# Kernel optimization log

Measured on AMD Instinct MI355X. Metric: run time of the kernel, lower is better.

Reference implementation:

```python
import jax, jax.numpy as jnp
import numpy as np

B, N, D_IN, D_OUT = 4, 2048, 1024, 1024


def setup_inputs() -> dict:
    key = jax.random.key(0)
    k0, k1, k2, k3 = jax.random.split(key, 4)
    x = jax.random.normal(k0, (B, N, D_IN), dtype=jnp.float32)
    # torch Linear weight is [out, in]; store transposed [in, out] for x @ W
    W_query = jax.random.normal(k1, (D_IN, D_OUT), dtype=jnp.float32) * (D_IN ** -0.5)
    W_key = jax.random.normal(k2, (D_IN, D_OUT), dtype=jnp.float32) * (D_IN ** -0.5)
    W_value = jax.random.normal(k3, (D_IN, D_OUT), dtype=jnp.float32) * (D_IN ** -0.5)
    return {"x": x, "W_query": W_query, "W_key": W_key, "W_value": W_value}


def reference(x, W_query, W_key, W_value):
    # x: [B, N, D_IN]
    num_tokens = x.shape[1]
    embed_dim = x.shape[2]  # NB: original scales by INPUT embed dim
    q = jnp.einsum('bnd,de->bne', x, W_query)  # [B, N, D_OUT]
    k = jnp.einsum('bnd,de->bne', x, W_key)
    v = jnp.einsum('bnd,de->bne', x, W_value)
    scores = jnp.einsum('bqe,bke->bqk', q, k)  # [B, N, N]
    idx = jnp.arange(num_tokens)
    causal_mask = idx[None, :] > idx[:, None]  # True above diagonal
    scores = jnp.where(causal_mask[None, :, :], -jnp.inf, scores)
    scale = jnp.asarray(embed_dim, scores.dtype) ** 0.5
    attn = jax.nn.softmax(scores / scale, axis=-1)  # dropout p=0 (eval)
    context = jnp.einsum('bqk,bke->bqe', attn, v)  # [B, N, D_OUT]
    return context
```

## Files before the change

### kernel.cpp

```cpp
#include <hip/hip_runtime.h>


typedef __attribute__((ext_vector_type(8))) _Float16 half8;
typedef __attribute__((ext_vector_type(4))) _Float16 half4v;
typedef __attribute__((ext_vector_type(4))) float floatx4;

#define AS1 __attribute__((address_space(1)))
#define AS3 __attribute__((address_space(3)))

__device__ __forceinline__ void load16_lds(void* lds, const void* g) {
  __builtin_amdgcn_global_load_lds((AS1 void*)g, (AS3 void*)lds, 16, 0, 0);
}


__global__ __launch_bounds__(256)
void conv_f32_f16(const float* __restrict__ in, _Float16* __restrict__ out,
                  float* __restrict__ l) {
  if (blockIdx.x < 8192) {
    const int i = (blockIdx.x * 256 + threadIdx.x) << 2;
    float4 v = *(const float4*)(in + i);
    half4v o = { (_Float16)v.x, (_Float16)v.y, (_Float16)v.z, (_Float16)v.w };
    *(half4v*)(out + i) = o;
  } else {
    const int i = ((blockIdx.x - 8192) * 256 + threadIdx.x) << 2;
    *(float4*)(l + i) = float4{0.f, 0.f, 0.f, 0.f};
  }
}

__global__ __launch_bounds__(256)
void transpose_w(const float* __restrict__ W0, const float* __restrict__ W1,
                 const float* __restrict__ W2, _Float16* __restrict__ Wt) {
  const float* W = blockIdx.z == 0 ? W0 : (blockIdx.z == 1 ? W1 : W2);
  _Float16* out = Wt + (long long)blockIdx.z * 1048576;
  __shared__ _Float16 t[32][33];
  const int tx = threadIdx.x, ty = threadIdx.y;
  const int n0 = blockIdx.x << 5, k0 = blockIdx.y << 5;
#pragma unroll
  for (int i = 0; i < 4; ++i)
    t[ty + i * 8][tx] = (_Float16)W[(long long)(k0 + ty + i * 8) * 1024 + n0 + tx];
  __syncthreads();
#pragma unroll
  for (int i = 0; i < 4; ++i)
    out[(long long)(n0 + ty + i * 8) * 1024 + k0 + tx] = t[tx][ty + i * 8];
}

__global__ __launch_bounds__(256)
void gemm_qkv(const _Float16* __restrict__ A, const _Float16* __restrict__ B,
              _Float16* __restrict__ Q, _Float16* __restrict__ Kh,
              _Float16* __restrict__ Vt) {
  const int bm = blockIdx.y, bn = blockIdx.x;
  const _Float16* Ab = A + (long long)bm * 128 * 1024;
  const _Float16* Bb = B + (long long)bn * 128 * 1024;

  __shared__ _Float16 As[128][64];
  __shared__ _Float16 Bs[128][64];

  const int tid = threadIdx.x;
  const int wave = tid >> 6, lane = tid & 63;
  const int quad = lane >> 4, lr = lane & 15;
  const int wm = (wave >> 1) << 6, wn = (wave & 1) << 6;
  const int srow = lane >> 3;
  const int goff = ((lane & 7) ^ srow) << 3;

  floatx4 acc[4][4] = {};
  const _Float16* ga = Ab + (long long)(wave * 8 + srow) * 1024 + goff;
  const _Float16* gb = Bb + (long long)(wave * 8 + srow) * 1024 + goff;

  for (int k0 = 0; k0 < 1024; k0 += 64) {
    __syncthreads();
#pragma unroll
    for (int c = 0; c < 4; ++c) {
      load16_lds(&As[wave * 8 + 32 * c][0], ga + c * 32 * 1024);
      load16_lds(&Bs[wave * 8 + 32 * c][0], gb + c * 32 * 1024);
    }
    ga += 64; gb += 64;
    __syncthreads();

#pragma unroll
    for (int kk = 0; kk < 2; ++kk) {
      half8 af[4], bf[4];
#pragma unroll
      for (int i = 0; i < 4; ++i) {
        const int ra = wm + (i << 4) + lr;
        const int rb = wn + (i << 4) + lr;
        af[i] = *(const half8*)&As[ra][(((kk << 2) + quad) ^ (ra & 7)) << 3];
        bf[i] = *(const half8*)&Bs[rb][(((kk << 2) + quad) ^ (rb & 7)) << 3];
      }
#pragma unroll
      for (int i = 0; i < 4; ++i)
#pragma unroll
        for (int j = 0; j < 4; ++j)
          acc[i][j] = __builtin_amdgcn_mfma_f32_16x16x32_f16(af[i], bf[j], acc[i][j], 0, 0, 0);
    }
  }

  const int colb = bn * 128 + wn + lr;
  const int rowb = bm * 128 + wm + (quad << 2);

  if (bn < 16) {
    _Float16* C = (bn < 8) ? Q : Kh;
    const int cb = colb & 1023;
#pragma unroll
    for (int i = 0; i < 4; ++i)
#pragma unroll
      for (int j = 0; j < 4; ++j)
#pragma unroll
        for (int r = 0; r < 4; ++r)
          C[(long long)(rowb + (i << 4) + r) * 1024 + cb + (j << 4)] =
              (_Float16)acc[i][j][r];
  } else {
    const int b = rowb >> 11;
    const int tb = rowb & 2047;
#pragma unroll
    for (int i = 0; i < 4; ++i) {
      const int tok = tb + (i << 4);
#pragma unroll
      for (int j = 0; j < 4; ++j) {
        const int d = (colb & 1023) + (j << 4);
        half4v v = { (_Float16)acc[i][j][0], (_Float16)acc[i][j][1],
                     (_Float16)acc[i][j][2], (_Float16)acc[i][j][3] };
        *(half4v*)&Vt[(long long)b * 2097152 + (long long)d * 2048 + tok] = v;
      }
    }
  }
}

__global__ __launch_bounds__(256)
void gemm_s_exp(const _Float16* __restrict__ Q, const _Float16* __restrict__ Kh,
                _Float16* __restrict__ P, float* __restrict__ l) {
  int t = blockIdx.x;
  const int bz = blockIdx.y;
  int bm = 0;
  for (;;) { const int c = (bm >> 2) + 1; if (t < c) break; t -= c; ++bm; }
  const int bn = t;

  const _Float16* Ab = Q  + (long long)bz * 2097152 + (long long)bm * 64 * 1024;
  const _Float16* Bb = Kh + (long long)bz * 2097152 + (long long)bn * 256 * 1024;
  const int nmaxl = bm * 64 + 63 - bn * 256;

  __shared__ _Float16 As[64][64];
  __shared__ _Float16 Bs[256][64];

  const int tid = threadIdx.x;
  const int wave = tid >> 6, lane = tid & 63;
  const int quad = lane >> 4, lr = lane & 15;
  const int srow = lane >> 3;
  const int goff = ((lane & 7) ^ srow) << 3;

  floatx4 acc[4][4] = {};
  const _Float16* ga = Ab + (long long)(wave * 16 + srow) * 1024 + goff;
  const _Float16* gb = Bb + (long long)(wave * 64 + srow) * 1024 + goff;

  for (int k0 = 0; k0 < 1024; k0 += 64) {
    __syncthreads();
    load16_lds(&As[wave * 16][0],     ga);
    load16_lds(&As[wave * 16 + 8][0], ga + 8 * 1024);
#pragma unroll
    for (int c = 0; c < 8; ++c)
      if (wave * 64 + 8 * c <= nmaxl)
        load16_lds(&Bs[wave * 64 + 8 * c][0], gb + c * 8 * 1024);
    ga += 64; gb += 64;
    __syncthreads();

#pragma unroll
    for (int kk = 0; kk < 2; ++kk) {
      half8 af[4], bf[4];
#pragma unroll
      for (int i = 0; i < 4; ++i) {
        const int ra = (i << 4) + lr;
        af[i] = *(const half8*)&As[ra][(((kk << 2) + quad) ^ (ra & 7)) << 3];
      }
#pragma unroll
      for (int j = 0; j < 4; ++j)
        if (wave * 64 + (j << 4) <= nmaxl) {
          const int rb = wave * 64 + (j << 4) + lr;
          bf[j] = *(const half8*)&Bs[rb][(((kk << 2) + quad) ^ (rb & 7)) << 3];
        }
#pragma unroll
      for (int i = 0; i < 4; ++i)
#pragma unroll
        for (int j = 0; j < 4; ++j)
          if (wave * 64 + (j << 4) <= nmaxl)
            acc[i][j] = __builtin_amdgcn_mfma_f32_16x16x32_f16(af[i], bf[j], acc[i][j], 0, 0, 0);
    }
  }

  const int n0 = bn * 256 + wave * 64;
  const int rowq = bm * 64 + (quad << 2);
  _Float16* Pb = P + (long long)bz * 4194304;
  const float scl = 0.03125f;

  float rs[4][4];
#pragma unroll
  for (int i = 0; i < 4; ++i)
#pragma unroll
    for (int r = 0; r < 4; ++r) rs[i][r] = 0.f;

#pragma unroll
  for (int j = 0; j < 4; ++j)
    if (wave * 64 + (j << 4) <= nmaxl) {
      const int kcol = n0 + (j << 4) + lr;
#pragma unroll
      for (int i = 0; i < 4; ++i)
#pragma unroll
        for (int r = 0; r < 4; ++r) {
          const int q = rowq + (i << 4) + r;
          const float p = (kcol <= q) ? __expf(acc[i][j][r] * scl) : 0.f;
          Pb[(long long)q * 2048 + kcol] = (_Float16)p;
          rs[i][r] += p;
        }
    }

#pragma unroll
  for (int i = 0; i < 4; ++i)
#pragma unroll
    for (int r = 0; r < 4; ++r) {
#pragma unroll
      for (int off = 1; off < 16; off <<= 1)
        rs[i][r] += __shfl_xor(rs[i][r], off);
    }
  if (lr == 0) {
    float* lb = l + bz * 2048;
#pragma unroll
    for (int i = 0; i < 4; ++i)
#pragma unroll
      for (int r = 0; r < 4; ++r)
        atomicAdd(&lb[rowq + (i << 4) + r], rs[i][r]);
  }
}

__global__ __launch_bounds__(256)
void gemm_pv(const _Float16* __restrict__ P, const _Float16* __restrict__ Vt,
             const float* __restrict__ l, float* __restrict__ out) {
  const int bn = blockIdx.x, bz = blockIdx.z;
  const int bm = 31 - blockIdx.y;
  const int Keff = 64 * (bm + 1);

  const _Float16* Ab = P  + (long long)bz * 4194304 + (long long)bm * 64 * 2048;
  const _Float16* Bb = Vt + (long long)bz * 2097152 + (long long)bn * 256 * 2048;

  __shared__ _Float16 As[64][64];
  __shared__ _Float16 Bs[256][64];

  const int tid = threadIdx.x;
  const int wave = tid >> 6, lane = tid & 63;
  const int quad = lane >> 4, lr = lane & 15;
  const int srow = lane >> 3;
  const int goff = ((lane & 7) ^ srow) << 3;

  floatx4 acc[4][4] = {};
  const _Float16* ga = Ab + (long long)(wave * 16 + srow) * 2048 + goff;
  const _Float16* gb = Bb + (long long)(wave * 64 + srow) * 2048 + goff;

  for (int k0 = 0; k0 < Keff; k0 += 64) {
    __syncthreads();
    load16_lds(&As[wave * 16][0],     ga);
    load16_lds(&As[wave * 16 + 8][0], ga + 8 * 2048);
#pragma unroll
    for (int c = 0; c < 8; ++c)
      load16_lds(&Bs[wave * 64 + 8 * c][0], gb + c * 8 * 2048);
    ga += 64; gb += 64;
    __syncthreads();

#pragma unroll
    for (int kk = 0; kk < 2; ++kk) {
      half8 af[4], bf[4];
#pragma unroll
      for (int i = 0; i < 4; ++i) {
        const int ra = (i << 4) + lr;
        af[i] = *(const half8*)&As[ra][(((kk << 2) + quad) ^ (ra & 7)) << 3];
      }
#pragma unroll
      for (int j = 0; j < 4; ++j) {
        const int rb = wave * 64 + (j << 4) + lr;
        bf[j] = *(const half8*)&Bs[rb][(((kk << 2) + quad) ^ (rb & 7)) << 3];
      }
#pragma unroll
      for (int i = 0; i < 4; ++i)
#pragma unroll
        for (int j = 0; j < 4; ++j)
          acc[i][j] = __builtin_amdgcn_mfma_f32_16x16x32_f16(af[i], bf[j], acc[i][j], 0, 0, 0);
    }
  }

  const int d0 = bn * 256 + wave * 64;
  const int rowq = bm * 64 + (quad << 2);
  const float* lb = l + bz * 2048;
  float* Cb = out + (long long)bz * 2097152;

  float linv[4][4];
#pragma unroll
  for (int i = 0; i < 4; ++i)
#pragma unroll
    for (int r = 0; r < 4; ++r)
      linv[i][r] = 1.0f / lb[rowq + (i << 4) + r];

#pragma unroll
  for (int i = 0; i < 4; ++i)
#pragma unroll
    for (int j = 0; j < 4; ++j)
#pragma unroll
      for (int r = 0; r < 4; ++r)
        Cb[(long long)(rowq + (i << 4) + r) * 1024 + d0 + (j << 4) + lr] =
            acc[i][j][r] * linv[i][r];
}


extern "C" void kernel_launch(void* const* d_in, const int* in_sizes, int n_in,
                              void* d_out, int out_size, void* d_ws, size_t ws_size,
                              hipStream_t stream) {
  const float* x  = (const float*)d_in[0];
  const float* Wq = (const float*)d_in[1];
  const float* Wk = (const float*)d_in[2];
  const float* Wv = (const float*)d_in[3];
  float* out = (float*)d_out;

  char* ws = (char*)d_ws;
  _Float16* xh = (_Float16*)(ws);
  _Float16* Wt = (_Float16*)(ws + 16777216);
  _Float16* Q  = (_Float16*)(ws + 23068672);
  _Float16* Kh = (_Float16*)(ws + 39845888);
  _Float16* Vt = (_Float16*)(ws + 56623104);
  _Float16* P  = (_Float16*)(ws + 73400320);
  float*    l  = (float*)   (ws + 106954752);

  conv_f32_f16<<<8200, 256, 0, stream>>>(x, xh, l);
  transpose_w<<<dim3(32, 32, 3), dim3(32, 8), 0, stream>>>(Wq, Wk, Wv, Wt);

  gemm_qkv<<<dim3(24, 64), 256, 0, stream>>>(xh, Wt, Q, Kh, Vt);

  gemm_s_exp<<<dim3(144, 4), 256, 0, stream>>>(Q, Kh, P, l);

  gemm_pv<<<dim3(4, 32, 4), 256, 0, stream>>>(P, Vt, l, out);
}
```

Baseline: 252.0 us.

## Double-buffer LDS tiles with K=32 stages in QK and PV GEMMs

Both attention GEMM kernels now split the shared-memory tiles into two buffers of K=32 and issue the next stage's direct-to-LDS global loads before computing on the current one. The aim is to overlap global memory latency with MFMA work and to cut the two barriers per iteration down to one. The swizzle pattern changes to suit 32-wide rows. The trade-off is twice as many loop iterations, each doing half the MFMA work. There is also a risk that the single barrier does not order the asynchronous LDS loads correctly without an explicit vmcnt wait.

```diff
diff --git a/kernel.cpp b/kernel.cpp
--- a/kernel.cpp
+++ b/kernel.cpp
@@ -138,51 +138,52 @@
   const _Float16* Bb = Kh + (long long)bz * 2097152 + (long long)bn * 256 * 1024;
   const int nmaxl = bm * 64 + 63 - bn * 256;
 
-  __shared__ _Float16 As[64][64];
-  __shared__ _Float16 Bs[256][64];
+  __shared__ _Float16 As[2][64][32];
+  __shared__ _Float16 Bs[2][256][32];
 
   const int tid = threadIdx.x;
   const int wave = tid >> 6, lane = tid & 63;
   const int quad = lane >> 4, lr = lane & 15;
-  const int srow = lane >> 3;
-  const int goff = ((lane & 7) ^ srow) << 3;
+  const int srow = lane >> 2;
+  const int goff = ((lane & 3) ^ ((srow >> 1) & 3)) << 3;
+
+  const _Float16* ga = Ab + (long long)(16 * wave + srow) * 1024 + goff;
+  const _Float16* gb = Bb + (long long)(64 * wave + srow) * 1024 + goff;
 
   floatx4 acc[4][4] = {};
-  const _Float16* ga = Ab + (long long)(wave * 16 + srow) * 1024 + goff;
-  const _Float16* gb = Bb + (long long)(wave * 64 + srow) * 1024 + goff;
-
-  for (int k0 = 0; k0 < 1024; k0 += 64) {
+
+  auto stage = [&](int buf, int kof) {
+    load16_lds(&As[buf][16 * wave][0], ga + kof);
+#pragma unroll
+    for (int c = 0; c < 4; ++c)
+      if (64 * wave + 16 * c <= nmaxl)
+        load16_lds(&Bs[buf][64 * wave + 16 * c][0], gb + 16 * c * 1024 + kof);
+  };
+
+  stage(0, 0);
+  for (int it = 0; it < 32; ++it) {
     __syncthreads();
-    load16_lds(&As[wave * 16][0],     ga);
-    load16_lds(&As[wave * 16 + 8][0], ga + 8 * 1024);
-#pragma unroll
-    for (int c = 0; c < 8; ++c)
-      if (wave * 64 + 8 * c <= nmaxl)
-        load16_lds(&Bs[wave * 64 + 8 * c][0], gb + c * 8 * 1024);
-    ga += 64; gb += 64;
-    __syncthreads();
-
-#pragma unroll
-    for (int kk = 0; kk < 2; ++kk) {
-      half8 af[4], bf[4];
-#pragma unroll
-      for (int i = 0; i < 4; ++i) {
-        const int ra = (i << 4) + lr;
-        af[i] = *(const half8*)&As[ra][(((kk << 2) + quad) ^ (ra & 7)) << 3];
+    if (it + 1 < 32) stage((it + 1) & 1, (it + 1) * 32);
+    const int buf = it & 1;
+
+    half8 af[4], bf[4];
+#pragma unroll
+    for (int i = 0; i < 4; ++i) {
+      const int ra = (i << 4) + lr;
+      af[i] = *(const half8*)&As[buf][ra][(quad ^ ((ra >> 1) & 3)) << 3];
+    }
+#pragma unroll
+    for (int j = 0; j < 4; ++j)
+      if (64 * wave + (j << 4) <= nmaxl) {
+        const int rb = 64 * wave + (j << 4) + lr;
+        bf[j] = *(const half8*)&Bs[buf][rb][(quad ^ ((rb >> 1) & 3)) << 3];
       }
 #pragma unroll
+    for (int i = 0; i < 4; ++i)
+#pragma unroll
       for (int j = 0; j < 4; ++j)
-        if (wave * 64 + (j << 4) <= nmaxl) {
-          const int rb = wave * 64 + (j << 4) + lr;
-          bf[j] = *(const half8*)&Bs[rb][(((kk << 2) + quad) ^ (rb & 7)) << 3];
-        }
-#pragma unroll
-      for (int i = 0; i < 4; ++i)
-#pragma unroll
-        for (int j = 0; j < 4; ++j)
-          if (wave * 64 + (j << 4) <= nmaxl)
-            acc[i][j] = __builtin_amdgcn_mfma_f32_16x16x32_f16(af[i], bf[j], acc[i][j], 0, 0, 0);
-    }
+        if (64 * wave + (j << 4) <= nmaxl)
+          acc[i][j] = __builtin_amdgcn_mfma_f32_16x16x32_f16(af[i], bf[j], acc[i][j], 0, 0, 0);
   }
 
   const int n0 = bn * 256 + wave * 64;
@@ -234,53 +235,54 @@
              const float* __restrict__ l, float* __restrict__ out) {
   const int bn = blockIdx.x, bz = blockIdx.z;
   const int bm = 31 - blockIdx.y;
-  const int Keff = 64 * (bm + 1);
+  const int niter = 2 * (bm + 1);
 
   const _Float16* Ab = P  + (long long)bz * 4194304 + (long long)bm * 64 * 2048;
   const _Float16* Bb = Vt + (long long)bz * 2097152 + (long long)bn * 256 * 2048;
 
-  __shared__ _Float16 As[64][64];
-  __shared__ _Float16 Bs[256][64];
+  __shared__ _Float16 As[2][64][32];
+  __shared__ _Float16 Bs[2][256][32];
 
   const int tid = threadIdx.x;
   const int wave = tid >> 6, lane = tid & 63;
   const int quad = lane >> 4, lr = lane & 15;
-  const int srow = lane >> 3;
-  const int goff = ((lane & 7) ^ srow) << 3;
+  const int srow = lane >> 2;
+  const int goff = ((lane & 3) ^ ((srow >> 1) & 3)) << 3;
+
+  const _Float16* ga = Ab + (long long)(16 * wave + srow) * 2048 + goff;
+  const _Float16* gb = Bb + (long long)(64 * wave + srow) * 2048 + goff;
 
   floatx4 acc[4][4] = {};
-  const _Float16* ga = Ab + (long long)(wave * 16 + srow) * 2048 + goff;
-  const _Float16* gb = Bb + (long long)(wave * 64 + srow) * 2048 + goff;
-
-  for (int k0 = 0; k0 < Keff; k0 += 64) {
+
+  auto stage = [&](int buf, int kof) {
+    load16_lds(&As[buf][16 * wave][0], ga + kof);
+#pragma unroll
+    for (int c = 0; c < 4; ++c)
+      load16_lds(&Bs[buf][64 * wave + 16 * c][0], gb + 16 * c * 2048 + kof);
+  };
+
+  stage(0, 0);
+  for (int it = 0; it < niter; ++it) {
     __syncthreads();
-    load16_lds(&As[wave * 16][0],     ga);
-    load16_lds(&As[wave * 16 + 8][0], ga + 8 * 2048);
-#pragma unroll
-    for (int c = 0; c < 8; ++c)
-      load16_lds(&Bs[wave * 64 + 8 * c][0], gb + c * 8 * 2048);
-    ga += 64; gb += 64;
-    __syncthreads();
-
-#pragma unroll
-    for (int kk = 0; kk < 2; ++kk) {
-      half8 af[4], bf[4];
-#pragma unroll
-      for (int i = 0; i < 4; ++i) {
-        const int ra = (i << 4) + lr;
-        af[i] = *(const half8*)&As[ra][(((kk << 2) + quad) ^ (ra & 7)) << 3];
-      }
-#pragma unroll
-      for (int j = 0; j < 4; ++j) {
-        const int rb = wave * 64 + (j << 4) + lr;
-        bf[j] = *(const half8*)&Bs[rb][(((kk << 2) + quad) ^ (rb & 7)) << 3];
-      }
-#pragma unroll
-      for (int i = 0; i < 4; ++i)
-#pragma unroll
-        for (int j = 0; j < 4; ++j)
-          acc[i][j] = __builtin_amdgcn_mfma_f32_16x16x32_f16(af[i], bf[j], acc[i][j], 0, 0, 0);
-    }
+    if (it + 1 < niter) stage((it + 1) & 1, (it + 1) * 32);
+    const int buf = it & 1;
+
+    half8 af[4], bf[4];
+#pragma unroll
+    for (int i = 0; i < 4; ++i) {
+      const int ra = (i << 4) + lr;
+      af[i] = *(const half8*)&As[buf][ra][(quad ^ ((ra >> 1) & 3)) << 3];
+    }
+#pragma unroll
+    for (int j = 0; j < 4; ++j) {
+      const int rb = 64 * wave + (j << 4) + lr;
+      bf[j] = *(const half8*)&Bs[buf][rb][(quad ^ ((rb >> 1) & 3)) << 3];
+    }
+#pragma unroll
+    for (int i = 0; i < 4; ++i)
+#pragma unroll
+      for (int j = 0; j < 4; ++j)
+        acc[i][j] = __builtin_amdgcn_mfma_f32_16x16x32_f16(af[i], bf[j], acc[i][j], 0, 0, 0);
   }
 
   const int d0 = bn * 256 + wave * 64;
```

After: 270.3 us. 1.07x slower.

## Retile score and PV GEMMs to square 128x128 blocks with 2x2 wave layout

Applied to the files above, without the earlier changes.

Both attention GEMMs move from 64x256 block tiles with one wave per 64-column strip to 128x128 tiles split into a 2x2 grid of waves. Each wave now holds a 64x64 output sub-tile. The aim is a better balance of LDS loads between the A and B operands and more operand reuse per byte loaded. The trade-off is coarser causal skipping: the per-wave masked-tile pruning in the score kernel is removed, so diagonal blocks compute some fully masked work, and the PV kernel has fewer, larger blocks.

```diff
diff --git a/kernel.cpp b/kernel.cpp
--- a/kernel.cpp
+++ b/kernel.cpp
@@ -129,36 +129,35 @@
 void gemm_s_exp(const _Float16* __restrict__ Q, const _Float16* __restrict__ Kh,
                 _Float16* __restrict__ P, float* __restrict__ l) {
   int t = blockIdx.x;
+  int bm = 0;
+  for (;;) { const int c = bm + 1; if (t < c) break; t -= c; ++bm; }
+  const int bn = t;
   const int bz = blockIdx.y;
-  int bm = 0;
-  for (;;) { const int c = (bm >> 2) + 1; if (t < c) break; t -= c; ++bm; }
-  const int bn = t;
-
-  const _Float16* Ab = Q  + (long long)bz * 2097152 + (long long)bm * 64 * 1024;
-  const _Float16* Bb = Kh + (long long)bz * 2097152 + (long long)bn * 256 * 1024;
-  const int nmaxl = bm * 64 + 63 - bn * 256;
-
-  __shared__ _Float16 As[64][64];
-  __shared__ _Float16 Bs[256][64];
+
+  const _Float16* Ab = Q  + (long long)bz * 2097152 + (long long)bm * 128 * 1024;
+  const _Float16* Bb = Kh + (long long)bz * 2097152 + (long long)bn * 128 * 1024;
+
+  __shared__ _Float16 As[128][64];
+  __shared__ _Float16 Bs[128][64];
 
   const int tid = threadIdx.x;
   const int wave = tid >> 6, lane = tid & 63;
   const int quad = lane >> 4, lr = lane & 15;
+  const int wm = (wave >> 1) << 6, wn = (wave & 1) << 6;
   const int srow = lane >> 3;
   const int goff = ((lane & 7) ^ srow) << 3;
 
   floatx4 acc[4][4] = {};
-  const _Float16* ga = Ab + (long long)(wave * 16 + srow) * 1024 + goff;
-  const _Float16* gb = Bb + (long long)(wave * 64 + srow) * 1024 + goff;
+  const _Float16* ga = Ab + (long long)(wave * 8 + srow) * 1024 + goff;
+  const _Float16* gb = Bb + (long long)(wave * 8 + srow) * 1024 + goff;
 
   for (int k0 = 0; k0 < 1024; k0 += 64) {
     __syncthreads();
-    load16_lds(&As[wave * 16][0],     ga);
-    load16_lds(&As[wave * 16 + 8][0], ga + 8 * 1024);
-#pragma unroll
-    for (int c = 0; c < 8; ++c)
-      if (wave * 64 + 8 * c <= nmaxl)
-        load16_lds(&Bs[wave * 64 + 8 * c][0], gb + c * 8 * 1024);
+#pragma unroll
+    for (int c = 0; c < 4; ++c) {
+      load16_lds(&As[wave * 8 + 32 * c][0], ga + c * 32 * 1024);
+      load16_lds(&Bs[wave * 8 + 32 * c][0], gb + c * 32 * 1024);
+    }
     ga += 64; gb += 64;
     __syncthreads();
 
@@ -167,26 +166,21 @@
       half8 af[4], bf[4];
 #pragma unroll
       for (int i = 0; i < 4; ++i) {
-        const int ra = (i << 4) + lr;
+        const int ra = wm + (i << 4) + lr;
+        const int rb = wn + (i << 4) + lr;
         af[i] = *(const half8*)&As[ra][(((kk << 2) + quad) ^ (ra & 7)) << 3];
-      }
-#pragma unroll
-      for (int j = 0; j < 4; ++j)
-        if (wave * 64 + (j << 4) <= nmaxl) {
-          const int rb = wave * 64 + (j << 4) + lr;
-          bf[j] = *(const half8*)&Bs[rb][(((kk << 2) + quad) ^ (rb & 7)) << 3];
-        }
+        bf[i] = *(const half8*)&Bs[rb][(((kk << 2) + quad) ^ (rb & 7)) << 3];
+      }
 #pragma unroll
       for (int i = 0; i < 4; ++i)
 #pragma unroll
         for (int j = 0; j < 4; ++j)
-          if (wave * 64 + (j << 4) <= nmaxl)
-            acc[i][j] = __builtin_amdgcn_mfma_f32_16x16x32_f16(af[i], bf[j], acc[i][j], 0, 0, 0);
-    }
-  }
-
-  const int n0 = bn * 256 + wave * 64;
-  const int rowq = bm * 64 + (quad << 2);
+          acc[i][j] = __builtin_amdgcn_mfma_f32_16x16x32_f16(af[i], bf[j], acc[i][j], 0, 0, 0);
+    }
+  }
+
+  const int colb = bn * 128 + wn + lr;
+  const int rowb = bm * 128 + wm + (quad << 2);
   _Float16* Pb = P + (long long)bz * 4194304;
   const float scl = 0.03125f;
 
@@ -197,19 +191,17 @@
     for (int r = 0; r < 4; ++r) rs[i][r] = 0.f;
 
 #pragma unroll
-  for (int j = 0; j < 4; ++j)
-    if (wave * 64 + (j << 4) <= nmaxl) {
-      const int kcol = n0 + (j << 4) + lr;
-#pragma unroll
-      for (int i = 0; i < 4; ++i)
-#pragma unroll
-        for (int r = 0; r < 4; ++r) {
-          const int q = rowq + (i << 4) + r;
-          const float p = (kcol <= q) ? __expf(acc[i][j][r] * scl) : 0.f;
-          Pb[(long long)q * 2048 + kcol] = (_Float16)p;
-          rs[i][r] += p;
-        }
-    }
+  for (int i = 0; i < 4; ++i)
+#pragma unroll
+    for (int j = 0; j < 4; ++j)
+#pragma unroll
+      for (int r = 0; r < 4; ++r) {
+        const int q = rowb + (i << 4) + r;
+        const int kcol = colb + (j << 4);
+        const float pv = (kcol <= q) ? __expf(acc[i][j][r] * scl) : 0.f;
+        Pb[(long long)q * 2048 + kcol] = (_Float16)pv;
+        rs[i][r] += pv;
+      }
 
 #pragma unroll
   for (int i = 0; i < 4; ++i)
@@ -225,40 +217,42 @@
     for (int i = 0; i < 4; ++i)
 #pragma unroll
       for (int r = 0; r < 4; ++r)
-        atomicAdd(&lb[rowq + (i << 4) + r], rs[i][r]);
+        atomicAdd(&lb[rowb + (i << 4) + r], rs[i][r]);
   }
 }
 
 __global__ __launch_bounds__(256)
 void gemm_pv(const _Float16* __restrict__ P, const _Float16* __restrict__ Vt,
              const float* __restrict__ l, float* __restrict__ out) {
-  const int bn = blockIdx.x, bz = blockIdx.z;
-  const int bm = 31 - blockIdx.y;
-  const int Keff = 64 * (bm + 1);
-
-  const _Float16* Ab = P  + (long long)bz * 4194304 + (long long)bm * 64 * 2048;
-  const _Float16* Bb = Vt + (long long)bz * 2097152 + (long long)bn * 256 * 2048;
-
-  __shared__ _Float16 As[64][64];
-  __shared__ _Float16 Bs[256][64];
+  const int dn = blockIdx.x;
+  const int bm = 15 - blockIdx.y;
+  const int bz = blockIdx.z;
+  const int Keff = 128 * (bm + 1);
+
+  const _Float16* Ab = P  + (long long)bz * 4194304 + (long long)bm * 128 * 2048;
+  const _Float16* Bb = Vt + (long long)bz * 2097152 + (long long)dn * 128 * 2048;
+
+  __shared__ _Float16 As[128][64];
+  __shared__ _Float16 Bs[128][64];
 
   const int tid = threadIdx.x;
   const int wave = tid >> 6, lane = tid & 63;
   const int quad = lane >> 4, lr = lane & 15;
+  const int wm = (wave >> 1) << 6, wn = (wave & 1) << 6;
   const int srow = lane >> 3;
   const int goff = ((lane & 7) ^ srow) << 3;
 
   floatx4 acc[4][4] = {};
-  const _Float16* ga = Ab + (long long)(wave * 16 + srow) * 2048 + goff;
-  const _Float16* gb = Bb + (long long)(wave * 64 + srow) * 2048 + goff;
+  const _Float16* ga = Ab + (long long)(wave * 8 + srow) * 2048 + goff;
+  const _Float16* gb = Bb + (long long)(wave * 8 + srow) * 2048 + goff;
 
   for (int k0 = 0; k0 < Keff; k0 += 64) {
     __syncthreads();
-    load16_lds(&As[wave * 16][0],     ga);
-    load16_lds(&As[wave * 16 + 8][0], ga + 8 * 2048);
-#pragma unroll
-    for (int c = 0; c < 8; ++c)
-      load16_lds(&Bs[wave * 64 + 8 * c][0], gb + c * 8 * 2048);
+#pragma unroll
+    for (int c = 0; c < 4; ++c) {
+      load16_lds(&As[wave * 8 + 32 * c][0], ga + (long long)c * 32 * 2048);
+      load16_lds(&Bs[wave * 8 + 32 * c][0], gb + (long long)c * 32 * 2048);
+    }
     ga += 64; gb += 64;
     __syncthreads();
 
@@ -267,13 +261,10 @@
       half8 af[4], bf[4];
 #pragma unroll
       for (int i = 0; i < 4; ++i) {
-        const int ra = (i << 4) + lr;
+        const int ra = wm + (i << 4) + lr;
+        const int rb = wn + (i << 4) + lr;
         af[i] = *(const half8*)&As[ra][(((kk << 2) + quad) ^ (ra & 7)) << 3];
-      }
-#pragma unroll
-      for (int j = 0; j < 4; ++j) {
-        const int rb = wave * 64 + (j << 4) + lr;
-        bf[j] = *(const half8*)&Bs[rb][(((kk << 2) + quad) ^ (rb & 7)) << 3];
+        bf[i] = *(const half8*)&Bs[rb][(((kk << 2) + quad) ^ (rb & 7)) << 3];
       }
 #pragma unroll
       for (int i = 0; i < 4; ++i)
@@ -283,8 +274,8 @@
     }
   }
 
-  const int d0 = bn * 256 + wave * 64;
-  const int rowq = bm * 64 + (quad << 2);
+  const int colb = dn * 128 + wn + lr;
+  const int rowb = bm * 128 + wm + (quad << 2);
   const float* lb = l + bz * 2048;
   float* Cb = out + (long long)bz * 2097152;
 
@@ -293,7 +284,7 @@
   for (int i = 0; i < 4; ++i)
 #pragma unroll
     for (int r = 0; r < 4; ++r)
-      linv[i][r] = 1.0f / lb[rowq + (i << 4) + r];
+      linv[i][r] = 1.0f / lb[rowb + (i << 4) + r];
 
 #pragma unroll
   for (int i = 0; i < 4; ++i)
@@ -301,7 +292,7 @@
     for (int j = 0; j < 4; ++j)
 #pragma unroll
       for (int r = 0; r < 4; ++r)
-        Cb[(long long)(rowq + (i << 4) + r) * 1024 + d0 + (j << 4) + lr] =
+        Cb[(long long)(rowb + (i << 4) + r) * 1024 + colb + (j << 4)] =
             acc[i][j][r] * linv[i][r];
 }
 
@@ -329,7 +320,7 @@
 
   gemm_qkv<<<dim3(24, 64), 256, 0, stream>>>(xh, Wt, Q, Kh, Vt);
 
-  gemm_s_exp<<<dim3(144, 4), 256, 0, stream>>>(Q, Kh, P, l);
-
-  gemm_pv<<<dim3(4, 32, 4), 256, 0, stream>>>(P, Vt, l, out);
-}
+  gemm_s_exp<<<dim3(136, 4), 256, 0, stream>>>(Q, Kh, P, l);
+
+  gemm_pv<<<dim3(8, 16, 4), 256, 0, stream>>>(P, Vt, l, out);
+}
```

New measurement: 250.1 us. Within noise of the previous version (-0.8%).
